# Performance work log

Hardware: AMD Instinct MI355X
Metric: run time of the kernel (lower is better)

Reference implementation:

```python
import jax, jax.numpy as jnp
import numpy as np

SLOPE = 0.01   # torch LeakyReLU default negative_slope
TASK_TYPE = 2
N, E = 50000, 800000
IN, EMB, OUT, EF = 128, 128, 128, 64


def leaky(x):
    return jnp.where(x >= 0, x, SLOPE * x)


def setup_inputs() -> dict:
    key = jax.random.key(0)
    ks = jax.random.split(key, 12)
    nf = jax.random.normal(ks[0], (N, IN), jnp.float32)
    ef = jax.random.normal(ks[1], (E, EF), jnp.float32)
    src = jax.random.randint(ks[2], (E,), 0, N)
    dst = jax.random.randint(ks[3], (E,), 0, N)
    ntype = jax.random.randint(ks[4], (N,), 0, 4)
    # layer dims: (in, out) per GNNLayer
    dims = [(IN, EMB), (EMB, EMB), (EMB, OUT)]
    inp = {"nf": nf, "ef": ef, "src": src, "dst": dst, "ntype": ntype}
    for i, (di, do) in enumerate(dims):
        inp[f"W_edge_{i}"] = jax.random.normal(ks[5 + i], (2 * di + EF, do), jnp.float32) / np.sqrt(2 * di + EF)
        inp[f"W_node_{i}"] = jax.random.normal(ks[8 + i], (di + do, do), jnp.float32) / np.sqrt(di + do)
    return inp


def gnn_layer(nf, ef, We, Wn, src, dst, active, recv):
    # message: concat(src_nf, dst_nf, ef) -> Linear(no bias) -> LeakyReLU, only on edges from task nodes
    m_in = jnp.concatenate([nf[src], nf[dst], ef], axis=-1)   # [E, 2*di+EF]
    msg = leaky(m_in @ We) * active[:, None]                  # [E, do]
    # reduce: sum messages at destination nodes
    red = jax.ops.segment_sum(msg, dst, num_segments=nf.shape[0])  # [N, do]
    # apply: concat(nf, red_msg) -> Linear(no bias) -> LeakyReLU; only receiving nodes updated (others zero, DGL default)
    out = leaky(jnp.concatenate([nf, red], axis=-1) @ Wn) * recv[:, None]
    return out


def reference(nf, ef, W_edge_0, W_edge_1, W_edge_2, W_node_0, W_node_1, W_node_2, src, dst, ntype):
    active = (ntype[src] == TASK_TYPE).astype(nf.dtype)       # edges emitted by push(u=task_nodes)
    recv = (jax.ops.segment_sum(active, dst, num_segments=nf.shape[0]) > 0).astype(nf.dtype)
    Wes = [W_edge_0, W_edge_1, W_edge_2]
    Wns = [W_node_0, W_node_1, W_node_2]
    h = nf
    for We, Wn in zip(Wes, Wns):
        h = gnn_layer(h, ef, We, Wn, src, dst, active, recv)  # residual=False
    return h
```

## Files before the change

kernel.cpp:

```cpp
#include <hip/hip_runtime.h>

typedef unsigned short u16;
typedef short s16x8 __attribute__((ext_vector_type(8)));
typedef float f32x4 __attribute__((ext_vector_type(4)));

#define SLOPE 0.01f
#define EPB 64

__device__ __forceinline__ float leaky(float x) { return x >= 0.f ? x : SLOPE * x; }

__device__ __forceinline__ u16 f2b(float f) {
    union { float f; unsigned u; } v; v.f = f;
    unsigned r = v.u + 0x7FFFu + ((v.u >> 16) & 1u);
    return (u16)(r >> 16);
}
__device__ __forceinline__ float b2f(u16 b) {
    union { unsigned u; float f; } v; v.u = ((unsigned)b) << 16; return v.f;
}

__global__ __launch_bounds__(256) void k_init(
    const int* __restrict__ src, const int* __restrict__ dst,
    const int* __restrict__ ntype, int* __restrict__ deg,
    float* __restrict__ recvf, int* __restrict__ tflag, int E, int N)
{
    int i = blockIdx.x * 256 + threadIdx.x;
    if (i < E) {
        if (ntype[src[i]] == 2) {
            int d = dst[i];
            atomicAdd(&deg[d], 1);
            recvf[d] = 1.0f;
        }
    } else {
        int j = i - E;
        if (j < N) tflag[j] = (ntype[j] == 2) ? 1 : 0;
    }
}

__global__ __launch_bounds__(256) void k_scan1(
    const int* __restrict__ deg, const int* __restrict__ tflag,
    int* __restrict__ bsum, int* __restrict__ bsum2, int n)
{
    __shared__ int s[256];
    const int* v = blockIdx.y ? tflag : deg;
    int* out = blockIdx.y ? bsum2 : bsum;
    int i = blockIdx.x * 256 + threadIdx.x;
    s[threadIdx.x] = (i < n) ? v[i] : 0;
    __syncthreads();
    for (int o = 128; o > 0; o >>= 1) {
        if (threadIdx.x < o) s[threadIdx.x] += s[threadIdx.x + o];
        __syncthreads();
    }
    if (threadIdx.x == 0) out[blockIdx.x] = s[0];
}

__global__ __launch_bounds__(256) void k_scan2(
    int* __restrict__ bsum, int* __restrict__ bsum2, int nb,
    int* __restrict__ cntp, int* __restrict__ tcntp)
{
    __shared__ int s[256];
    int* arr = blockIdx.x ? bsum2 : bsum;
    int* tot = blockIdx.x ? tcntp : cntp;
    int v = (threadIdx.x < nb) ? arr[threadIdx.x] : 0;
    s[threadIdx.x] = v;
    __syncthreads();
    for (int o = 1; o < 256; o <<= 1) {
        int x = (threadIdx.x >= o) ? s[threadIdx.x - o] : 0;
        __syncthreads();
        s[threadIdx.x] += x;
        __syncthreads();
    }
    if (threadIdx.x < nb) arr[threadIdx.x] = s[threadIdx.x] - v;
    if (threadIdx.x == 255) *tot = s[255];
}

__global__ __launch_bounds__(256) void k_scan3(
    const int* __restrict__ deg, const int* __restrict__ tflag,
    const int* __restrict__ bsum, const int* __restrict__ bsum2,
    int* __restrict__ cursor, int* __restrict__ trank,
    int* __restrict__ tlist, int n)
{
    __shared__ int s[256];
    const int sel = blockIdx.y;
    const int* v = sel ? tflag : deg;
    const int* bexcl = sel ? bsum2 : bsum;
    int i = blockIdx.x * 256 + threadIdx.x;
    int x = (i < n) ? v[i] : 0;
    s[threadIdx.x] = x;
    __syncthreads();
    for (int o = 1; o < 256; o <<= 1) {
        int y = (threadIdx.x >= o) ? s[threadIdx.x - o] : 0;
        __syncthreads();
        s[threadIdx.x] += y;
        __syncthreads();
    }
    if (i < n) {
        int off = bexcl[blockIdx.x] + s[threadIdx.x] - x;
        if (sel) {
            trank[i] = off;
            if (x) tlist[off] = i;
        } else {
            cursor[i] = off;
        }
    }
}

__global__ __launch_bounds__(256) void k_scatter_pos(
    const int* __restrict__ src, const int* __restrict__ dst,
    const int* __restrict__ ntype, const int* __restrict__ trank,
    int* __restrict__ cursor, int* __restrict__ eS,
    int* __restrict__ sSg, int* __restrict__ dSg, int E)
{
    int e = blockIdx.x * 256 + threadIdx.x;
    if (e < E) {
        int s = src[e];
        if (ntype[s] == 2) {
            int d = dst[e];
            int p = atomicAdd(&cursor[d], 1);
            eS[p] = e; sSg[p] = trank[s]; dSg[p] = d;
        }
    }
}

__global__ __launch_bounds__(256) void k_efgather(
    const float* __restrict__ ef, const int* __restrict__ eS,
    const int* __restrict__ cntp, u16* __restrict__ efS)
{
    const int cnt = *cntp;
    const int b0 = blockIdx.x * 64;
    if (b0 >= cnt) return;
    const int t = threadIdx.x;
    #pragma unroll
    for (int pz = 0; pz < 4; ++pz) {
        int idx = t + pz * 256;
        int edge = idx >> 4, f4 = idx & 15;
        int p = b0 + edge;
        if (p < cnt) {
            float4 v = *(const float4*)(ef + (size_t)eS[p] * 64 + f4 * 4);
            ushort4 o;
            o.x = f2b(v.x); o.y = f2b(v.y); o.z = f2b(v.z); o.w = f2b(v.w);
            *(ushort4*)(efS + (size_t)p * 64 + f4 * 4) = o;
        }
    }
}

__global__ __launch_bounds__(256) void k_prep(
    const float* __restrict__ nf, u16* __restrict__ hb0, int n4,
    const float* __restrict__ We0, const float* __restrict__ We1,
    const float* __restrict__ We2, const float* __restrict__ Wn0,
    const float* __restrict__ Wn1, const float* __restrict__ Wn2,
    u16* __restrict__ WTe, u16* __restrict__ WTn, u16* __restrict__ WTef)
{
    int i = blockIdx.x * 256 + threadIdx.x;
    if (i < n4) {
        float4 v = ((const float4*)nf)[i];
        ushort4 o;
        o.x = f2b(v.x); o.y = f2b(v.y); o.z = f2b(v.z); o.w = f2b(v.w);
        ((ushort4*)hb0)[i] = o;
        return;
    }
    int j = i - n4;
    if (j >= 3 * 73728) return;
    int l = j / 73728;
    int idx = j - l * 73728;
    const float* We = (l == 0) ? We0 : (l == 1) ? We1 : We2;
    const float* Wn = (l == 0) ? Wn0 : (l == 1) ? Wn1 : Wn2;
    if (idx < 32768) {
        int sel = idx >> 14, jj = idx & 16383;
        int k = jj >> 7, n = jj & 127;
        WTe[(size_t)l * 32768 + sel * 16384 + n * 128 + k] = f2b(We[sel * 16384 + jj]);
    } else if (idx < 65536) {
        int jj = idx - 32768;
        int k = jj >> 7, n = jj & 127;
        WTn[(size_t)l * 32768 + n * 256 + k] = f2b(Wn[jj]);
    } else {
        int jj = idx - 65536;
        int k = jj >> 7, n = jj & 127;
        WTef[(size_t)l * 8192 + n * 64 + k] = f2b(We[32768 + jj]);
    }
}

__global__ __launch_bounds__(256) void k_gemm_T2(
    const u16* __restrict__ A, const u16* __restrict__ WTe_l,
    u16* __restrict__ Tsrc, u16* __restrict__ Tdst,
    const int* __restrict__ tlist, const int* __restrict__ tcntp, int Nfull)
{
    __shared__ u16 As[128][72];
    __shared__ u16 Bs[128][72];
    const int sel = blockIdx.y;
    const int M = sel ? Nfull : *tcntp;
    const int m0 = blockIdx.x * 128;
    if (m0 >= M) return;
    const u16* WT = WTe_l + sel * 16384;
    u16* T = sel ? Tdst : Tsrc;
    const int t = threadIdx.x;
    const int w = t >> 6, lane = t & 63, wm = w >> 1, wn = w & 1;
    f32x4 acc[4][4] = {};

    const int row = t >> 1, koff = (t & 1) * 32;
    const int gm_s = m0 + row;
    int arow = gm_s;
    if (!sel && gm_s < M) arow = tlist[gm_s];

    for (int kt = 0; kt < 128; kt += 64) {
        #pragma unroll
        for (int j = 0; j < 4; ++j) {
            int4 va = make_int4(0, 0, 0, 0);
            if (gm_s < M) va = *(const int4*)(A + (size_t)arow * 128 + kt + koff + j * 8);
            *(int4*)&As[row][koff + j * 8] = va;
            *(int4*)&Bs[row][koff + j * 8] =
                *(const int4*)(WT + (size_t)row * 128 + kt + koff + j * 8);
        }
        __syncthreads();
        #pragma unroll
        for (int kf = 0; kf < 2; ++kf) {
            s16x8 a[4], b[4];
            #pragma unroll
            for (int mi = 0; mi < 4; ++mi)
                a[mi] = *(const s16x8*)&As[wm * 64 + mi * 16 + (lane & 15)][kf * 32 + (lane >> 4) * 8];
            #pragma unroll
            for (int ni = 0; ni < 4; ++ni)
                b[ni] = *(const s16x8*)&Bs[wn * 64 + ni * 16 + (lane & 15)][kf * 32 + (lane >> 4) * 8];
            #pragma unroll
            for (int mi = 0; mi < 4; ++mi)
                #pragma unroll
                for (int ni = 0; ni < 4; ++ni)
                    acc[mi][ni] = __builtin_amdgcn_mfma_f32_16x16x32_bf16(
                        a[mi], b[ni], acc[mi][ni], 0, 0, 0);
        }
        __syncthreads();
    }
    const int lr = (lane >> 4) * 4, lc = lane & 15;
    #pragma unroll
    for (int mi = 0; mi < 4; ++mi) {
        #pragma unroll
        for (int r = 0; r < 4; ++r) {
            int gm = m0 + wm * 64 + mi * 16 + lr + r;
            if (gm < M) {
                #pragma unroll
                for (int ni = 0; ni < 4; ++ni)
                    T[(size_t)gm * 128 + wn * 64 + ni * 16 + lc] = f2b(acc[mi][ni][r]);
            }
        }
    }
}

__global__ __launch_bounds__(256) void k_gemm_node(
    const u16* __restrict__ H, float* __restrict__ R,
    const u16* __restrict__ WT, const float* __restrict__ recvf,
    u16* __restrict__ O16, float* __restrict__ O32, int fin, int M)
{
    __shared__ u16 As[128][72];
    __shared__ u16 Bs[128][72];
    const int t = threadIdx.x;
    const int m0 = blockIdx.x * 128;
    const int w = t >> 6, lane = t & 63, wm = w >> 1, wn = w & 1;
    f32x4 acc[4][4] = {};

    const int row = t >> 1, koff = (t & 1) * 32;
    const int gm_s = m0 + row;

    for (int kt = 0; kt < 256; kt += 64) {
        if (kt < 128) {
            #pragma unroll
            for (int j = 0; j < 4; ++j) {
                int4 va = make_int4(0, 0, 0, 0);
                if (gm_s < M) va = *(const int4*)(H + (size_t)gm_s * 128 + kt + koff + j * 8);
                *(int4*)&As[row][koff + j * 8] = va;
            }
        } else {
            #pragma unroll
            for (int j = 0; j < 8; ++j) {
                float4 v = make_float4(0.f, 0.f, 0.f, 0.f);
                if (gm_s < M) {
                    float* rp = R + (size_t)gm_s * 128 + (kt - 128) + koff + j * 4;
                    v = *(const float4*)rp;
                    *(float4*)rp = make_float4(0.f, 0.f, 0.f, 0.f);
                }
                ushort4 o;
                o.x = f2b(v.x); o.y = f2b(v.y); o.z = f2b(v.z); o.w = f2b(v.w);
                *(ushort4*)&As[row][koff + j * 4] = o;
            }
        }
        #pragma unroll
        for (int j = 0; j < 4; ++j)
            *(int4*)&Bs[row][koff + j * 8] =
                *(const int4*)(WT + (size_t)row * 256 + kt + koff + j * 8);
        __syncthreads();
        #pragma unroll
        for (int kf = 0; kf < 2; ++kf) {
            s16x8 a[4], b[4];
            #pragma unroll
            for (int mi = 0; mi < 4; ++mi)
                a[mi] = *(const s16x8*)&As[wm * 64 + mi * 16 + (lane & 15)][kf * 32 + (lane >> 4) * 8];
            #pragma unroll
            for (int ni = 0; ni < 4; ++ni)
                b[ni] = *(const s16x8*)&Bs[wn * 64 + ni * 16 + (lane & 15)][kf * 32 + (lane >> 4) * 8];
            #pragma unroll
            for (int mi = 0; mi < 4; ++mi)
                #pragma unroll
                for (int ni = 0; ni < 4; ++ni)
                    acc[mi][ni] = __builtin_amdgcn_mfma_f32_16x16x32_bf16(
                        a[mi], b[ni], acc[mi][ni], 0, 0, 0);
        }
        __syncthreads();
    }
    const int lr = (lane >> 4) * 4, lc = lane & 15;
    #pragma unroll
    for (int mi = 0; mi < 4; ++mi) {
        #pragma unroll
        for (int r = 0; r < 4; ++r) {
            int gm = m0 + wm * 64 + mi * 16 + lr + r;
            if (gm < M) {
                float rv = recvf[gm];
                #pragma unroll
                for (int ni = 0; ni < 4; ++ni) {
                    float val = leaky(acc[mi][ni][r]) * rv;
                    size_t o = (size_t)gm * 128 + wn * 64 + ni * 16 + lc;
                    if (fin) O32[o] = val;
                    else     O16[o] = f2b(val);
                }
            }
        }
    }
}

__global__ __launch_bounds__(512) void k_edge(
    const u16* __restrict__ efS, const u16* __restrict__ WTef,
    const u16* __restrict__ Tsrc, const u16* __restrict__ Tdst,
    const int* __restrict__ sSg, const int* __restrict__ dSg,
    const int* __restrict__ cntp, float* __restrict__ red)
{
    __shared__ u16 Ms[64][136];
    __shared__ int sS[EPB], sD[EPB];

    const int t = threadIdx.x;
    const int cnt = *cntp;
    const int b0 = blockIdx.x * EPB;
    if (b0 >= cnt) return;

    if (t < EPB) {
        int p = b0 + t;
        sS[t] = (p < cnt) ? sSg[p] : -1;
        sD[t] = (p < cnt) ? dSg[p] : -1;
    }

    const int w = t >> 6, lane = t & 63;
    const int lo = lane & 15, q = lane >> 4;

    if (w < 4) {
        const int ei = w * 16 + lo;
        const int p = b0 + ei;
        f32x4 acc[8] = {};
        #pragma unroll
        for (int kf = 0; kf < 2; ++kf) {
            s16x8 b = {};
            if (p < cnt) b = *(const s16x8*)(efS + (size_t)p * 64 + kf * 32 + q * 8);
            #pragma unroll
            for (int mi = 0; mi < 8; ++mi) {
                s16x8 a = *(const s16x8*)(WTef + (size_t)(mi * 16 + lo) * 64 + kf * 32 + q * 8);
                acc[mi] = __builtin_amdgcn_mfma_f32_16x16x32_bf16(a, b, acc[mi], 0, 0, 0);
            }
        }
        #pragma unroll
        for (int mi = 0; mi < 8; ++mi) {
            ushort4 o;
            o.x = f2b(acc[mi][0]); o.y = f2b(acc[mi][1]);
            o.z = f2b(acc[mi][2]); o.w = f2b(acc[mi][3]);
            *(ushort4*)&Ms[ei][mi * 16 + q * 4] = o;
        }
    }
    __syncthreads();

    float a0 = 0.f, a1 = 0.f;
    int dprev = -1;
    float td0 = 0.f, td1 = 0.f;
    for (int ii = 0; ii < 8; ++ii) {
        int e2 = w * 8 + ii;
        if (b0 + e2 >= cnt) break;
        int d = sD[e2], s = sS[e2];
        if (d != dprev) {
            td0 = b2f(Tdst[(size_t)d * 128 + lane]);
            td1 = b2f(Tdst[(size_t)d * 128 + 64 + lane]);
            dprev = d;
        }
        float t0 = b2f(Tsrc[(size_t)s * 128 + lane]);
        float t1 = b2f(Tsrc[(size_t)s * 128 + 64 + lane]);
        a0 += leaky(b2f(Ms[e2][lane])      + t0 + td0);
        a1 += leaky(b2f(Ms[e2][64 + lane]) + t1 + td1);
        bool last = (ii == 7) || (b0 + e2 + 1 >= cnt) || (sD[e2 + 1] != d);
        if (last) {
            atomicAdd(red + (size_t)d * 128 + lane,      a0);
            atomicAdd(red + (size_t)d * 128 + 64 + lane, a1);
            a0 = 0.f; a1 = 0.f;
        }
    }
}

extern "C" void kernel_launch(void* const* d_in, const int* in_sizes, int n_in,
                              void* d_out, int out_size, void* d_ws, size_t ws_size,
                              hipStream_t stream)
{
    const float* nf    = (const float*)d_in[0];
    const float* ef    = (const float*)d_in[1];
    const int*   src   = (const int*)d_in[2];
    const int*   dst   = (const int*)d_in[3];
    const int*   ntype = (const int*)d_in[4];
    const float* We[3] = {(const float*)d_in[5], (const float*)d_in[7], (const float*)d_in[9]};
    const float* Wn[3] = {(const float*)d_in[6], (const float*)d_in[8], (const float*)d_in[10]};

    const int N = in_sizes[0] / 128;
    const int E = in_sizes[1] / 64;

    u16* Tsrc = (u16*)d_ws;
    u16* Tdst = Tsrc + (size_t)N * 128;
    u16* hb0  = Tdst + (size_t)N * 128;
    u16* hb1  = hb0 + (size_t)N * 128;
    u16* WTe  = hb1 + (size_t)N * 128;
    u16* WTn  = WTe + 3 * 32768;
    u16* WTef = WTn + 3 * 32768;
    u16* efS  = WTef + 3 * 8192;
    float* red   = (float*)(efS + (size_t)E * 64);
    float* recvf = red + (size_t)N * 128;
    int* deg    = (int*)(recvf + N);
    int* cursor = deg + N;
    int* tflag  = cursor + N;
    int* trank  = tflag + N;
    int* tlist  = trank + N;
    int* bsum   = tlist + N;
    int* bsum2  = bsum + 256;
    int* cntp   = bsum2 + 256;
    int* tcntp  = cntp + 4;
    int* eS     = tcntp + 4;
    int* sSg    = eS + E;
    int* dSg    = sSg + E;

    const int nb  = (N + 255) / 256;
    const int gEb = (E + 255) / 256;
    const int n4  = N * 128 / 4;

    hipMemsetAsync(recvf, 0, (size_t)N * 2 * sizeof(float), stream);
    hipMemsetAsync(red, 0, (size_t)N * 128 * sizeof(float), stream);

    k_init<<<(E + N + 255) / 256, 256, 0, stream>>>(src, dst, ntype, deg, recvf, tflag, E, N);
    k_scan1<<<dim3(nb, 2), 256, 0, stream>>>(deg, tflag, bsum, bsum2, N);
    k_scan2<<<2, 256, 0, stream>>>(bsum, bsum2, nb, cntp, tcntp);
    k_scan3<<<dim3(nb, 2), 256, 0, stream>>>(deg, tflag, bsum, bsum2, cursor, trank, tlist, N);
    k_scatter_pos<<<gEb, 256, 0, stream>>>(src, dst, ntype, trank, cursor, eS, sSg, dSg, E);
    k_efgather<<<(E + 63) / 64, 256, 0, stream>>>(ef, eS, cntp, efS);
    k_prep<<<(n4 + 3 * 73728 + 255) / 256, 256, 0, stream>>>(
        nf, hb0, n4, We[0], We[1], We[2], Wn[0], Wn[1], Wn[2], WTe, WTn, WTef);

    dim3 gG((N + 127) / 128);
    dim3 gT((N + 127) / 128, 2);
    int  gE = (E + EPB - 1) / EPB;

    const u16* hIn[3]  = {hb0, hb1, hb0};
    u16*       hOut[3] = {hb1, hb0, hb1};
    for (int l = 0; l < 3; ++l) {
        int fin = (l == 2);
        k_gemm_T2<<<gT, 256, 0, stream>>>(hIn[l], WTe + (size_t)l * 32768,
                                          Tsrc, Tdst, tlist, tcntp, N);
        k_edge<<<gE, 512, 0, stream>>>(efS, WTef + (size_t)l * 8192, Tsrc, Tdst,
                                       sSg, dSg, cntp, red);
        k_gemm_node<<<gG, 256, 0, stream>>>(hIn[l], red, WTn + (size_t)l * 32768,
                                            recvf, hOut[l], (float*)d_out, fin, N);
    }
}
```

Baseline: 364.2 us.

## Split edge kernel into message GEMM and atomic-free per-destination segmented reduce

Replaces the fused edge kernel, which used float atomics into a float32 reduction buffer, with two kernels. One computes the edge-feature projection into a bf16 message buffer, and the other does a wavefront-per-destination segmented sum over the CSR-sorted edges, reading Tdst once and writing a bf16 result with no atomics. It also drops the dSg array, the memset of the float reduction buffer, and the read-and-zero of that buffer in the node GEMM. In exchange it adds a full round trip of an E×128 bf16 message buffer through global memory per layer, plus an extra launch, and the reduced sum is now rounded to bf16 before the node GEMM.

```diff
diff --git a/kernel.cpp b/kernel.cpp
--- a/kernel.cpp
+++ b/kernel.cpp
@@ -108,7 +108,7 @@
     const int* __restrict__ src, const int* __restrict__ dst,
     const int* __restrict__ ntype, const int* __restrict__ trank,
     int* __restrict__ cursor, int* __restrict__ eS,
-    int* __restrict__ sSg, int* __restrict__ dSg, int E)
+    int* __restrict__ sSg, int E)
 {
     int e = blockIdx.x * 256 + threadIdx.x;
     if (e < E) {
@@ -116,7 +116,7 @@
         if (ntype[s] == 2) {
             int d = dst[e];
             int p = atomicAdd(&cursor[d], 1);
-            eS[p] = e; sSg[p] = trank[s]; dSg[p] = d;
+            eS[p] = e; sSg[p] = trank[s];
         }
     }
 }
@@ -244,8 +244,78 @@
     }
 }
 
+__global__ __launch_bounds__(256) void k_msg(
+    const u16* __restrict__ efS, const u16* __restrict__ WTef,
+    const int* __restrict__ cntp, u16* __restrict__ msgS)
+{
+    __shared__ u16 Ms[64][136];
+    const int cnt = *cntp;
+    const int b0 = blockIdx.x * EPB;
+    if (b0 >= cnt) return;
+    const int t = threadIdx.x;
+    const int w = t >> 6, lane = t & 63;
+    const int lo = lane & 15, q = lane >> 4;
+    const int ei = w * 16 + lo;
+    const int p = b0 + ei;
+
+    f32x4 acc[8] = {};
+    #pragma unroll
+    for (int kf = 0; kf < 2; ++kf) {
+        s16x8 b = {};
+        if (p < cnt) b = *(const s16x8*)(efS + (size_t)p * 64 + kf * 32 + q * 8);
+        #pragma unroll
+        for (int mi = 0; mi < 8; ++mi) {
+            s16x8 a = *(const s16x8*)(WTef + (size_t)(mi * 16 + lo) * 64 + kf * 32 + q * 8);
+            acc[mi] = __builtin_amdgcn_mfma_f32_16x16x32_bf16(a, b, acc[mi], 0, 0, 0);
+        }
+    }
+    #pragma unroll
+    for (int mi = 0; mi < 8; ++mi) {
+        ushort4 o;
+        o.x = f2b(acc[mi][0]); o.y = f2b(acc[mi][1]);
+        o.z = f2b(acc[mi][2]); o.w = f2b(acc[mi][3]);
+        *(ushort4*)&Ms[ei][mi * 16 + q * 4] = o;
+    }
+    __syncthreads();
+    #pragma unroll
+    for (int pz = 0; pz < 4; ++pz) {
+        int idx = t + pz * 256;
+        int row = idx >> 4, c8 = idx & 15;
+        int pp = b0 + row;
+        if (pp < cnt)
+            *(int4*)(msgS + (size_t)pp * 128 + c8 * 8) = *(const int4*)&Ms[row][c8 * 8];
+    }
+}
+
+__global__ __launch_bounds__(256) void k_reduce(
+    const u16* __restrict__ msgS, const u16* __restrict__ Tsrc,
+    const u16* __restrict__ Tdst, const int* __restrict__ sSg,
+    const int* __restrict__ deg, const int* __restrict__ segEnd,
+    u16* __restrict__ redb, int N)
+{
+    const int w = threadIdx.x >> 6, lane = threadIdx.x & 63;
+    const int d = blockIdx.x * 4 + w;
+    if (d >= N) return;
+    const int dg = deg[d];
+    if (dg == 0) return;
+    const int end = segEnd[d], beg = end - dg;
+
+    unsigned td = *(const unsigned*)(Tdst + (size_t)d * 128 + lane * 2);
+    const float td0 = b2f((u16)(td & 0xffff)), td1 = b2f((u16)(td >> 16));
+    float a0 = 0.f, a1 = 0.f;
+    for (int i = beg; i < end; ++i) {
+        int s = sSg[i];
+        unsigned m  = *(const unsigned*)(msgS + (size_t)i * 128 + lane * 2);
+        unsigned ts = *(const unsigned*)(Tsrc + (size_t)s * 128 + lane * 2);
+        a0 += leaky(b2f((u16)(m & 0xffff)) + b2f((u16)(ts & 0xffff)) + td0);
+        a1 += leaky(b2f((u16)(m >> 16))    + b2f((u16)(ts >> 16))    + td1);
+    }
+    unsigned out = (unsigned)f2b(a0) | ((unsigned)f2b(a1) << 16);
+    *(unsigned*)(redb + (size_t)d * 128 + lane * 2) = out;
+}
+
 __global__ __launch_bounds__(256) void k_gemm_node(
-    const u16* __restrict__ H, float* __restrict__ R,
+    const u16* __restrict__ H, const u16* __restrict__ R,
     const u16* __restrict__ WT, const float* __restrict__ recvf,
     u16* __restrict__ O16, float* __restrict__ O32, int fin, int M)
 {
@@ -260,31 +330,15 @@
     const int gm_s = m0 + row;
 
     for (int kt = 0; kt < 256; kt += 64) {
-        if (kt < 128) {
-            #pragma unroll
-            for (int j = 0; j < 4; ++j) {
-                int4 va = make_int4(0, 0, 0, 0);
-                if (gm_s < M) va = *(const int4*)(H + (size_t)gm_s * 128 + kt + koff + j * 8);
-                *(int4*)&As[row][koff + j * 8] = va;
-            }
-        } else {
-            #pragma unroll
-            for (int j = 0; j < 8; ++j) {
-                float4 v = make_float4(0.f, 0.f, 0.f, 0.f);
-                if (gm_s < M) {
-                    float* rp = R + (size_t)gm_s * 128 + (kt - 128) + koff + j * 4;
-                    v = *(const float4*)rp;
-                    *(float4*)rp = make_float4(0.f, 0.f, 0.f, 0.f);
-                }
-                ushort4 o;
-                o.x = f2b(v.x); o.y = f2b(v.y); o.z = f2b(v.z); o.w = f2b(v.w);
-                *(ushort4*)&As[row][koff + j * 4] = o;
-            }
-        }
-        #pragma unroll
-        for (int j = 0; j < 4; ++j)
+        const u16* Ap = (kt < 128) ? (H + kt) : (R + (kt - 128));
+        #pragma unroll
+        for (int j = 0; j < 4; ++j) {
+            int4 va = make_int4(0, 0, 0, 0);
+            if (gm_s < M) va = *(const int4*)(Ap + (size_t)gm_s * 128 + koff + j * 8);
+            *(int4*)&As[row][koff + j * 8] = va;
             *(int4*)&Bs[row][koff + j * 8] =
                 *(const int4*)(WT + (size_t)row * 256 + kt + koff + j * 8);
+        }
         __syncthreads();
         #pragma unroll
         for (int kf = 0; kf < 2; ++kf) {
@@ -324,78 +378,6 @@
     }
 }
 
-__global__ __launch_bounds__(512) void k_edge(
-    const u16* __restrict__ efS, const u16* __restrict__ WTef,
-    const u16* __restrict__ Tsrc, const u16* __restrict__ Tdst,
-    const int* __restrict__ sSg, const int* __restrict__ dSg,
-    const int* __restrict__ cntp, float* __restrict__ red)
-{
-    __shared__ u16 Ms[64][136];
-    __shared__ int sS[EPB], sD[EPB];
-
-    const int t = threadIdx.x;
-    const int cnt = *cntp;
-    const int b0 = blockIdx.x * EPB;
-    if (b0 >= cnt) return;
-
-    if (t < EPB) {
-        int p = b0 + t;
-        sS[t] = (p < cnt) ? sSg[p] : -1;
-        sD[t] = (p < cnt) ? dSg[p] : -1;
-    }
-
-    const int w = t >> 6, lane = t & 63;
-    const int lo = lane & 15, q = lane >> 4;
-
-    if (w < 4) {
-        const int ei = w * 16 + lo;
-        const int p = b0 + ei;
-        f32x4 acc[8] = {};
-        #pragma unroll
-        for (int kf = 0; kf < 2; ++kf) {
-            s16x8 b = {};
-            if (p < cnt) b = *(const s16x8*)(efS + (size_t)p * 64 + kf * 32 + q * 8);
-            #pragma unroll
-            for (int mi = 0; mi < 8; ++mi) {
-                s16x8 a = *(const s16x8*)(WTef + (size_t)(mi * 16 + lo) * 64 + kf * 32 + q * 8);
-                acc[mi] = __builtin_amdgcn_mfma_f32_16x16x32_bf16(a, b, acc[mi], 0, 0, 0);
-            }
-        }
-        #pragma unroll
-        for (int mi = 0; mi < 8; ++mi) {
-            ushort4 o;
-            o.x = f2b(acc[mi][0]); o.y = f2b(acc[mi][1]);
-            o.z = f2b(acc[mi][2]); o.w = f2b(acc[mi][3]);
-            *(ushort4*)&Ms[ei][mi * 16 + q * 4] = o;
-        }
-    }
-    __syncthreads();
-
-    float a0 = 0.f, a1 = 0.f;
-    int dprev = -1;
-    float td0 = 0.f, td1 = 0.f;
-    for (int ii = 0; ii < 8; ++ii) {
-        int e2 = w * 8 + ii;
-        if (b0 + e2 >= cnt) break;
-        int d = sD[e2], s = sS[e2];
-        if (d != dprev) {
-            td0 = b2f(Tdst[(size_t)d * 128 + lane]);
-            td1 = b2f(Tdst[(size_t)d * 128 + 64 + lane]);
-            dprev = d;
-        }
-        float t0 = b2f(Tsrc[(size_t)s * 128 + lane]);
-        float t1 = b2f(Tsrc[(size_t)s * 128 + 64 + lane]);
-        a0 += leaky(b2f(Ms[e2][lane])      + t0 + td0);
-        a1 += leaky(b2f(Ms[e2][64 + lane]) + t1 + td1);
-        bool last = (ii == 7) || (b0 + e2 + 1 >= cnt) || (sD[e2 + 1] != d);
-        if (last) {
-            atomicAdd(red + (size_t)d * 128 + lane,      a0);
-            atomicAdd(red + (size_t)d * 128 + 64 + lane, a1);
-            a0 = 0.f; a1 = 0.f;
-        }
-    }
-}
-
 extern "C" void kernel_launch(void* const* d_in, const int* in_sizes, int n_in,
                               void* d_out, int out_size, void* d_ws, size_t ws_size,
                               hipStream_t stream)
@@ -415,12 +397,13 @@
     u16* Tdst = Tsrc + (size_t)N * 128;
     u16* hb0  = Tdst + (size_t)N * 128;
     u16* hb1  = hb0 + (size_t)N * 128;
-    u16* WTe  = hb1 + (size_t)N * 128;
+    u16* redb = hb1 + (size_t)N * 128;
+    u16* WTe  = redb + (size_t)N * 128;
     u16* WTn  = WTe + 3 * 32768;
     u16* WTef = WTn + 3 * 32768;
     u16* efS  = WTef + 3 * 8192;
-    float* red   = (float*)(efS + (size_t)E * 64);
-    float* recvf = red + (size_t)N * 128;
+    u16* msgS = efS + (size_t)E * 64;
+    float* recvf = (float*)(msgS + (size_t)E * 128);
     int* deg    = (int*)(recvf + N);
     int* cursor = deg + N;
     int* tflag  = cursor + N;
@@ -432,20 +415,18 @@
     int* tcntp  = cntp + 4;
     int* eS     = tcntp + 4;
     int* sSg    = eS + E;
-    int* dSg    = sSg + E;
 
     const int nb  = (N + 255) / 256;
     const int gEb = (E + 255) / 256;
     const int n4  = N * 128 / 4;
 
     hipMemsetAsync(recvf, 0, (size_t)N * 2 * sizeof(float), stream);
-    hipMemsetAsync(red, 0, (size_t)N * 128 * sizeof(float), stream);
 
     k_init<<<(E + N + 255) / 256, 256, 0, stream>>>(src, dst, ntype, deg, recvf, tflag, E, N);
     k_scan1<<<dim3(nb, 2), 256, 0, stream>>>(deg, tflag, bsum, bsum2, N);
     k_scan2<<<2, 256, 0, stream>>>(bsum, bsum2, nb, cntp, tcntp);
     k_scan3<<<dim3(nb, 2), 256, 0, stream>>>(deg, tflag, bsum, bsum2, cursor, trank, tlist, N);
-    k_scatter_pos<<<gEb, 256, 0, stream>>>(src, dst, ntype, trank, cursor, eS, sSg, dSg, E);
+    k_scatter_pos<<<gEb, 256, 0, stream>>>(src, dst, ntype, trank, cursor, eS, sSg, E);
     k_efgather<<<(E + 63) / 64, 256, 0, stream>>>(ef, eS, cntp, efS);
     k_prep<<<(n4 + 3 * 73728 + 255) / 256, 256, 0, stream>>>(
         nf, hb0, n4, We[0], We[1], We[2], Wn[0], Wn[1], Wn[2], WTe, WTn, WTef);
@@ -453,6 +434,7 @@
     dim3 gG((N + 127) / 128);
     dim3 gT((N + 127) / 128, 2);
     int  gE = (E + EPB - 1) / EPB;
+    int  gR = (N + 3) / 4;
 
     const u16* hIn[3]  = {hb0, hb1, hb0};
     u16*       hOut[3] = {hb1, hb0, hb1};
@@ -460,9 +442,9 @@
         int fin = (l == 2);
         k_gemm_T2<<<gT, 256, 0, stream>>>(hIn[l], WTe + (size_t)l * 32768,
                                           Tsrc, Tdst, tlist, tcntp, N);
-        k_edge<<<gE, 512, 0, stream>>>(efS, WTef + (size_t)l * 8192, Tsrc, Tdst,
-                                       sSg, dSg, cntp, red);
-        k_gemm_node<<<gG, 256, 0, stream>>>(hIn[l], red, WTn + (size_t)l * 32768,
+        k_msg<<<gE, 256, 0, stream>>>(efS, WTef + (size_t)l * 8192, cntp, msgS);
+        k_reduce<<<gR, 256, 0, stream>>>(msgS, Tsrc, Tdst, sSg, deg, cursor, redb, N);
+        k_gemm_node<<<gG, 256, 0, stream>>>(hIn[l], redb, WTn + (size_t)l * 32768,
                                             recvf, hOut[l], (float*)d_out, fin, N);
     }
 }
```

Result: faster. 342.7 us (-5.9%).
